# Kernel optimization log

Hardware: AMD Instinct MI355X
Metric: run time of the kernel (lower is better)

Reference implementation:

```python
import jax, jax.numpy as jnp
import numpy as np

N_NODES = 100000
N_EDGES = 1600000
IN_DIM = 33
HID = 128
N_CLASSES = 10
N_GRAPHS = 128


def _glorot(key, shape):
    fan_in, fan_out = shape[0], shape[1]
    lim = (6.0 / (fan_in + fan_out)) ** 0.5
    return jax.random.uniform(key, shape, jnp.float32, -lim, lim)


def setup_inputs() -> dict:
    key = jax.random.key(0)
    ks = jax.random.split(key, 20)
    x = jax.random.normal(ks[0], (N_NODES, IN_DIM), jnp.float32)
    edge_index = jax.random.randint(ks[1], (2, N_EDGES), 0, N_NODES, jnp.int64)
    edge_w = jax.random.uniform(ks[2], (N_EDGES,), jnp.float32)
    batch = jnp.sort(jax.random.randint(ks[3], (N_NODES,), 0, N_GRAPHS, jnp.int64))
    p = {
        "We": _glorot(ks[4], (IN_DIM, HID)), "be": jnp.zeros((HID,), jnp.float32),
        "W1": _glorot(ks[5], (HID, HID)), "b1": jnp.zeros((HID,), jnp.float32),
        "W2": _glorot(ks[6], (HID, HID)), "b2": jnp.zeros((HID,), jnp.float32),
        "W3": _glorot(ks[7], (HID, HID)), "b3": jnp.zeros((HID,), jnp.float32),
        "W4": _glorot(ks[8], (HID, HID)), "b4": jnp.zeros((HID,), jnp.float32),
        "Wr1": _glorot(ks[9], (HID, HID // 2)), "br1": jnp.zeros((HID // 2,), jnp.float32),
        "Wr2": _glorot(ks[10], (HID // 2, HID // 4)), "br2": jnp.zeros((HID // 4,), jnp.float32),
        "Wr3": _glorot(ks[11], (HID // 4, N_CLASSES)),
    }
    return dict(x=x, edge_index=edge_index, edge_w=edge_w, batch=batch, **p)


def reference(x, edge_index, edge_w, batch,
              We, be, W1, b1, W2, b2, W3, b3, W4, b4,
              Wr1, br1, Wr2, br2, Wr3):
    N = x.shape[0]
    row, col = edge_index[0], edge_index[1]
    # PyG gcn_norm with add_self_loops=True: append (i,i) edges with weight 1
    loop = jnp.arange(N)
    row2 = jnp.concatenate([row, loop])
    col2 = jnp.concatenate([col, loop])
    w2 = jnp.concatenate([edge_w, jnp.ones((N,), edge_w.dtype)])
    deg = jax.ops.segment_sum(w2, col2, num_segments=N)  # in-degree incl. self-loop
    dinv = jnp.where(deg > 0, deg ** -0.5, 0.0)
    norm = dinv[row2] * w2 * dinv[col2]  # [E+N] symmetric normalization

    def conv(h, W, b):
        h = h @ W  # linear transform first (PyG GCNConv)
        msg = norm[:, None] * h[row2]  # gather + scale
        return jax.ops.segment_sum(msg, col2, num_segments=N) + b  # scatter-add to targets

    h = x @ We + be
    h = jax.nn.relu(conv(h, W1, b1))
    h = jax.nn.relu(conv(h, W2, b2))
    h = jax.nn.relu(conv(h, W3, b3))
    h = jax.nn.relu(conv(h, W4, b4))

    # global mean pool over graphs
    sums = jax.ops.segment_sum(h, batch, num_segments=N_GRAPHS)
    cnt = jax.ops.segment_sum(jnp.ones((N,), h.dtype), batch, num_segments=N_GRAPHS)
    pooled = sums / jnp.maximum(cnt, 1.0)[:, None]  # [G, HID]

    r = jax.nn.relu(pooled @ Wr1 + br1)
    r = jax.nn.relu(r @ Wr2 + br2)
    return r @ Wr3  # [G, n_classes]
```

## Files before the change

kernel.cpp:

```cpp
#include <hip/hip_runtime.h>
#include <hip/hip_bf16.h>

#define NN 100000
#define NE 1600000
#define IN_DIM 33
#define HID 128
#define NG 128
#define NCLS 10

using short8 = __attribute__((ext_vector_type(8))) short;
using floatx4 = __attribute__((ext_vector_type(4))) float;

static __device__ __forceinline__ size_t szmul(int a, int b) {
    return (size_t)a * (size_t)b;
}

static __device__ __forceinline__ unsigned short f2bf(float f) {
    unsigned u = __float_as_uint(f);
    u += 0x7fffu + ((u >> 16) & 1u);
    return (unsigned short)(u >> 16);
}
static __device__ __forceinline__ float bf_lo(unsigned u) { return __uint_as_float(u << 16); }
static __device__ __forceinline__ float bf_hi(unsigned u) { return __uint_as_float(u & 0xffff0000u); }

__global__ void k_init(int* bucket_cnt, int* bucket_fill, float* gsum) {
    int i = blockIdx.x * blockDim.x + threadIdx.x;
    if (i < 513) { bucket_cnt[i] = 0; bucket_fill[i] = 0; }
    if (i < NG * HID) gsum[i] = 0.0f;
}


__global__ __launch_bounds__(256) void k_bhist(const int* __restrict__ col,
                                               int* __restrict__ bucket_cnt, int e, int nbk) {
    __shared__ int hist[512];
    int tid = threadIdx.x;
    for (int i = tid; i < nbk; i += 256) hist[i] = 0;
    __syncthreads();
    for (int i = blockIdx.x * 256 + tid; i < e; i += 256 * 256)
        atomicAdd(&hist[col[i] >> 8], 1);
    __syncthreads();
    for (int i = tid; i < nbk; i += 256)
        if (hist[i]) atomicAdd(&bucket_cnt[i], hist[i]);
}

__global__ void k_scan_small(int* data, int nb) {
    __shared__ int s[512];
    int t = threadIdx.x;
    int v = (t < nb) ? data[t] : 0;
    s[t] = v;
    __syncthreads();
    for (int o = 1; o < 512; o <<= 1) {
        int a = (t >= o) ? s[t - o] : 0;
        __syncthreads();
        s[t] += a;
        __syncthreads();
    }
    if (t < nb) data[t] = s[t] - v;
    if (t == nb - 1) data[nb] = s[t];
}

__global__ __launch_bounds__(256) void k_bin_scatter(const int* __restrict__ row,
                                                     const int* __restrict__ col,
                                                     const float* __restrict__ w,
                                                     const int* __restrict__ bucket_base,
                                                     int* __restrict__ bucket_fill,
                                                     uint2* __restrict__ binned, int e, int nbk) {
    __shared__ int hist[512], rnk[512], basub[512];
    int tid = threadIdx.x;
    int c0 = blockIdx.x * 4096;
    for (int i = tid; i < nbk; i += 256) { hist[i] = 0; rnk[i] = 0; }
    __syncthreads();
    int myb[16]; unsigned myp[16]; unsigned myw[16];
#pragma unroll
    for (int u = 0; u < 16; ++u) {
        int idx = c0 + u * 256 + tid;
        int b = -1;
        if (idx < e) {
            int c = col[idx];
            int r = row[idx];
            myw[u] = __float_as_uint(w[idx]);
            b = c >> 8;
            myp[u] = ((unsigned)(c & 255) << 17) | (unsigned)r;
            atomicAdd(&hist[b], 1);
        }
        myb[u] = b;
    }
    __syncthreads();
    for (int i = tid; i < nbk; i += 256) {
        int c = hist[i];
        basub[i] = (c > 0) ? (bucket_base[i] + atomicAdd(&bucket_fill[i], c)) : 0;
    }
    __syncthreads();
#pragma unroll
    for (int u = 0; u < 16; ++u) {
        int b = myb[u];
        if (b >= 0) {
            int rk = atomicAdd(&rnk[b], 1);
            binned[basub[b] + rk] = make_uint2(myp[u], myw[u]);
        }
    }
}

__global__ __launch_bounds__(256) void k_bucket_cnt(const uint2* __restrict__ binned,
                                                    const int* __restrict__ bucket_base,
                                                    int* __restrict__ cnt,
                                                    float* __restrict__ wsum, int n) {
    __shared__ int c256[256];
    __shared__ float s256[256];
    int b = blockIdx.x, tid = threadIdx.x;
    c256[tid] = 0;
    s256[tid] = 0.0f;
    __syncthreads();
    int beg = bucket_base[b], end = bucket_base[b + 1];
    for (int e2 = beg + tid; e2 < end; e2 += 256) {
        uint2 rec = binned[e2];
        int lo = (rec.x >> 17) & 255;
        atomicAdd(&c256[lo], 1);
        atomicAdd(&s256[lo], __uint_as_float(rec.y));
    }
    __syncthreads();
    int node = b * 256 + tid;
    if (node < n) { cnt[node] = c256[tid]; wsum[node] = s256[tid]; }
}

__global__ void k_dinv(float* __restrict__ dinv, float* __restrict__ selfn, int n) {
    int i = blockIdx.x * blockDim.x + threadIdx.x;
    if (i >= n) return;
    float d = 1.0f + dinv[i];
    float di = (d > 0.0f) ? (1.0f / sqrtf(d)) : 0.0f;
    dinv[i] = di;
    selfn[i] = di * di;
}

#define SCAN_B 1024
__global__ void k_scan1(const int* __restrict__ cnt, int* __restrict__ rowptr,
                        int* __restrict__ bsums, int n) {
    __shared__ int s[SCAN_B];
    int t = threadIdx.x;
    int i = blockIdx.x * SCAN_B + t;
    int v = (i < n) ? cnt[i] : 0;
    s[t] = v;
    __syncthreads();
    for (int o = 1; o < SCAN_B; o <<= 1) {
        int a = (t >= o) ? s[t - o] : 0;
        __syncthreads();
        s[t] += a;
        __syncthreads();
    }
    if (i < n) rowptr[i] = s[t] - v;
    if (t == SCAN_B - 1) bsums[blockIdx.x] = s[t];
}

__global__ void k_scan3(int* rowptr, const int* __restrict__ bsums, int n, int etot) {
    int i = blockIdx.x * blockDim.x + threadIdx.x;
    if (i < n) rowptr[i] += bsums[i >> 10];
    else if (i == n) rowptr[n] = etot;
}

__global__ __launch_bounds__(256) void k_bucket_scatter(const uint2* __restrict__ binned,
                                                        const int* __restrict__ bucket_base,
                                                        const int* __restrict__ rowptr,
                                                        const float* __restrict__ dinv,
                                                        int2* __restrict__ csr, int n) {
    __shared__ int f256[256];
    int b = blockIdx.x, tid = threadIdx.x;
    f256[tid] = 0;
    __syncthreads();
    int beg = bucket_base[b], end = bucket_base[b + 1];
    for (int e2 = beg + tid; e2 < end; e2 += 256) {
        uint2 rec = binned[e2];
        int lo = (rec.x >> 17) & 255;
        int node = (b << 8) | lo;
        int src = rec.x & 0x1FFFF;
        float nw = dinv[src] * __uint_as_float(rec.y) * dinv[node];
        int pos = rowptr[node] + atomicAdd(&f256[lo], 1);
        csr[pos] = make_int2(src, __float_as_int(nw));
    }
    (void)n;
}

__global__ void k_combine(const float* __restrict__ We, const float* __restrict__ W1,
                          const float* __restrict__ be,
                          float* __restrict__ M, float* __restrict__ v) {
    int f = threadIdx.x;
    int k = blockIdx.x;
    if (k < IN_DIM) {
        float a = 0.0f;
#pragma unroll 8
        for (int j = 0; j < HID; ++j) a += We[k * HID + j] * W1[j * HID + f];
        M[k * HID + f] = a;
    } else {
        float a = 0.0f;
#pragma unroll 8
        for (int j = 0; j < HID; ++j) a += be[j] * W1[j * HID + f];
        v[f] = a;
    }
}

__global__ void k_wcast3(const float* __restrict__ W1, const float* __restrict__ W2,
                         const float* __restrict__ W3, unsigned short* __restrict__ Wt) {
    int k = blockIdx.x, c = threadIdx.x, l = blockIdx.y;
    const float* W = (l == 0) ? W1 : (l == 1) ? W2 : W3;
    Wt[((size_t)l * HID + c) * HID + k] = f2bf(W[k * HID + c]);
}

__global__ __launch_bounds__(256) void k_gemm_x(const float* __restrict__ x,
                                                const float* __restrict__ M,
                                                const float* __restrict__ v,
                                                unsigned short* __restrict__ tb, int n) {
    __shared__ float sX[32 * IN_DIM];
    int n0 = blockIdx.x * 32;
    int tid = threadIdx.x;
    int cnt = n - n0; if (cnt > 32) cnt = 32;
    for (int idx = tid; idx < cnt * IN_DIM; idx += 256)
        sX[idx] = x[szmul(n0, IN_DIM) + idx];
    __syncthreads();
    int f = tid & 127, g = tid >> 7;
    float Mc[IN_DIM];
#pragma unroll
    for (int k = 0; k < IN_DIM; ++k) Mc[k] = M[k * HID + f];
    float vf = v[f];
    int ndEnd = g * 16 + 16; if (ndEnd > cnt) ndEnd = cnt;
    for (int nd = g * 16; nd < ndEnd; ++nd) {
        float a = vf;
#pragma unroll
        for (int k = 0; k < IN_DIM; ++k) a += sX[nd * IN_DIM + k] * Mc[k];
        tb[szmul(n0 + nd, HID) + f] = f2bf(a);
    }
}

__global__ __launch_bounds__(256) void k_gemm_mfma(const unsigned short* __restrict__ A,
                                                   const unsigned short* __restrict__ Wt,
                                                   unsigned short* __restrict__ T, int n) {
    int wave = threadIdx.x >> 6;
    int lane = threadIdx.x & 63;
    int r = lane & 15, kg = lane >> 4;
    int row0 = blockIdx.x * 64 + wave * 16;
    int arow = row0 + r;
    short8 af[4];
#pragma unroll
    for (int kk = 0; kk < 4; ++kk) {
        if (arow < n)
            af[kk] = *reinterpret_cast<const short8*>(A + szmul(arow, HID) + kk * 32 + kg * 8);
        else
            af[kk] = short8{0, 0, 0, 0, 0, 0, 0, 0};
    }
    floatx4 acc[8];
#pragma unroll
    for (int ct = 0; ct < 8; ++ct) acc[ct] = floatx4{0.f, 0.f, 0.f, 0.f};
#pragma unroll
    for (int kk = 0; kk < 4; ++kk) {
#pragma unroll
        for (int ct = 0; ct < 8; ++ct) {
            short8 bf = *reinterpret_cast<const short8*>(
                Wt + (size_t)(ct * 16 + r) * HID + kk * 32 + kg * 8);
            acc[ct] = __builtin_amdgcn_mfma_f32_16x16x32_bf16(af[kk], bf, acc[ct], 0, 0, 0);
        }
    }
#pragma unroll
    for (int ct = 0; ct < 8; ++ct) {
#pragma unroll
        for (int reg = 0; reg < 4; ++reg) {
            int orow = row0 + kg * 4 + reg;
            if (orow < n)
                T[szmul(orow, HID) + ct * 16 + r] = f2bf(acc[ct][reg]);
        }
    }
}

__global__ __launch_bounds__(256) void k_aggregate(const uint4* __restrict__ tb,
                                                   const int* __restrict__ rowptr,
                                                   const int2* __restrict__ csr,
                                                   const float* __restrict__ selfn,
                                                   const float* __restrict__ bias,
                                                   uint4* __restrict__ hout, int n) {
    int i = (blockIdx.x * 256 + threadIdx.x) >> 4;
    if (i >= n) return;
    int p = threadIdx.x & 15;
    uint4 sv = tb[szmul(i, 16) + p];
    float sn = selfn[i];
    const float4* bp = reinterpret_cast<const float4*>(bias + p * 8);
    float4 b0 = bp[0], b1 = bp[1];
    float a0 = b0.x + sn * bf_lo(sv.x), a1 = b0.y + sn * bf_hi(sv.x);
    float a2 = b0.z + sn * bf_lo(sv.y), a3 = b0.w + sn * bf_hi(sv.y);
    float a4 = b1.x + sn * bf_lo(sv.z), a5 = b1.y + sn * bf_hi(sv.z);
    float a6 = b1.z + sn * bf_lo(sv.w), a7 = b1.w + sn * bf_hi(sv.w);
    int beg = rowptr[i], end = rowptr[i + 1];
#pragma unroll 4
    for (int j = beg; j < end; ++j) {
        int2 e = csr[j];
        float wj = __int_as_float(e.y);
        uint4 r = tb[szmul(e.x, 16) + p];
        a0 += wj * bf_lo(r.x); a1 += wj * bf_hi(r.x);
        a2 += wj * bf_lo(r.y); a3 += wj * bf_hi(r.y);
        a4 += wj * bf_lo(r.z); a5 += wj * bf_hi(r.z);
        a6 += wj * bf_lo(r.w); a7 += wj * bf_hi(r.w);
    }
    unsigned u0 = (unsigned)f2bf(fmaxf(a0, 0.f)) | ((unsigned)f2bf(fmaxf(a1, 0.f)) << 16);
    unsigned u1 = (unsigned)f2bf(fmaxf(a2, 0.f)) | ((unsigned)f2bf(fmaxf(a3, 0.f)) << 16);
    unsigned u2 = (unsigned)f2bf(fmaxf(a4, 0.f)) | ((unsigned)f2bf(fmaxf(a5, 0.f)) << 16);
    unsigned u3 = (unsigned)f2bf(fmaxf(a6, 0.f)) | ((unsigned)f2bf(fmaxf(a7, 0.f)) << 16);
    hout[szmul(i, 16) + p] = make_uint4(u0, u1, u2, u3);
}

__global__ void k_gcount_bs(const int* __restrict__ batch, int* gcnt, int n) {
    int g = threadIdx.x;
    if (g >= NG) return;
    int lo = 0, hi = n;
    while (lo < hi) { int mid = (lo + hi) >> 1; if (batch[mid] < g) lo = mid + 1; else hi = mid; }
    int start = lo;
    lo = 0; hi = n;
    while (lo < hi) { int mid = (lo + hi) >> 1; if (batch[mid] < g + 1) lo = mid + 1; else hi = mid; }
    gcnt[g] = lo - start;
}

__global__ __launch_bounds__(128) void k_pool(const unsigned short* __restrict__ h,
                                              const int* __restrict__ batch,
                                              float* gsum, int n) {
    int f = threadIdx.x;
    int i0 = blockIdx.x * 32;
    int i1 = min(i0 + 32, n);
    if (i0 >= n) return;
    float acc = 0.0f;
    int cur = batch[i0];
    for (int i = i0; i < i1; ++i) {
        int g = batch[i];
        if (g != cur) { atomicAdd(&gsum[cur * HID + f], acc); acc = 0.0f; cur = g; }
        acc += __uint_as_float((unsigned)h[szmul(i, HID) + f] << 16);
    }
    atomicAdd(&gsum[cur * HID + f], acc);
}

__global__ __launch_bounds__(128) void k_mlp(const float* __restrict__ gsum,
                                             const int* __restrict__ gcnt,
                                             const float* __restrict__ Wr1, const float* __restrict__ br1,
                                             const float* __restrict__ Wr2, const float* __restrict__ br2,
                                             const float* __restrict__ Wr3,
                                             float* __restrict__ out) {
    int g = blockIdx.x;
    int t = threadIdx.x;
    __shared__ float p[HID];
    __shared__ float r1[64];
    __shared__ float r2[32];
    float c = fmaxf((float)gcnt[g], 1.0f);
    p[t] = gsum[g * HID + t] / c;
    __syncthreads();
    if (t < 64) {
        float a = br1[t];
#pragma unroll 8
        for (int k = 0; k < HID; ++k) a += p[k] * Wr1[k * 64 + t];
        r1[t] = fmaxf(a, 0.0f);
    }
    __syncthreads();
    if (t < 32) {
        float a = br2[t];
#pragma unroll 8
        for (int k = 0; k < 64; ++k) a += r1[k] * Wr2[k * 32 + t];
        r2[t] = fmaxf(a, 0.0f);
    }
    __syncthreads();
    if (t < NCLS) {
        float a = 0.0f;
#pragma unroll
        for (int k = 0; k < 32; ++k) a += r2[k] * Wr3[k * NCLS + t];
        out[g * NCLS + t] = a;
    }
}

extern "C" void kernel_launch(void* const* d_in, const int* in_sizes, int n_in,
                              void* d_out, int out_size, void* d_ws, size_t ws_size,
                              hipStream_t stream) {
    const float* x     = (const float*)d_in[0];
    const int*   ei    = (const int*)d_in[1];
    const float* ew    = (const float*)d_in[2];
    const int*   batch = (const int*)d_in[3];
    const float* We  = (const float*)d_in[4];
    const float* be  = (const float*)d_in[5];
    const float* Wl[4] = { (const float*)d_in[6], (const float*)d_in[8],
                           (const float*)d_in[10], (const float*)d_in[12] };
    const float* bl[4] = { (const float*)d_in[7], (const float*)d_in[9],
                           (const float*)d_in[11], (const float*)d_in[13] };
    const float* Wr1 = (const float*)d_in[14];
    const float* br1 = (const float*)d_in[15];
    const float* Wr2 = (const float*)d_in[16];
    const float* br2 = (const float*)d_in[17];
    const float* Wr3 = (const float*)d_in[18];
    float* out = (float*)d_out;

    const int N = in_sizes[3];
    const int E = in_sizes[2];
    const int* row = ei;
    const int* col = ei + E;
    const int nbk = (N + 255) >> 8;

    char* w = (char*)d_ws;
    size_t off = 0;
    auto alloc = [&](size_t bytes) -> void* {
        void* p = w + off;
        off = (off + bytes + 255) & ~(size_t)255;
        return p;
    };
    float* dinv       = (float*)alloc((size_t)N * 4);
    float* selfn      = (float*)alloc((size_t)N * 4);
    int*   cnt        = (int*)  alloc((size_t)N * 4);
    int*   rowptr     = (int*)  alloc((size_t)(N + 1) * 4);
    int*   bsums      = (int*)  alloc(4096);
    int*   bucket_cnt = (int*)  alloc(513 * 4);
    int*   bucket_fill= (int*)  alloc(513 * 4);
    int2*  csr        = (int2*) alloc((size_t)E * 8);
    unsigned short* h  = (unsigned short*)alloc((size_t)N * HID * 2);
    unsigned short* tb = (unsigned short*)alloc((size_t)N * HID * 2);
    unsigned short* Wt = (unsigned short*)alloc((size_t)3 * HID * HID * 2);
    float* M          = (float*)alloc((size_t)IN_DIM * HID * 4);
    float* vbe        = (float*)alloc((size_t)HID * 4);
    float* gsum       = (float*)alloc((size_t)NG * HID * 4);
    int*   gcnt       = (int*)  alloc((size_t)NG * 4);
    uint2* binned     = (uint2*)tb;
    (void)ws_size;

    auto cdiv = [](int a, int b) { return (a + b - 1) / b; };

    k_init<<<64, 256, 0, stream>>>(bucket_cnt, bucket_fill, gsum);
    k_bhist<<<256, 256, 0, stream>>>(col, bucket_cnt, E, nbk);
    k_scan_small<<<1, 512, 0, stream>>>(bucket_cnt, nbk);
    k_bin_scatter<<<cdiv(E, 4096), 256, 0, stream>>>(row, col, ew, bucket_cnt,
                                                     bucket_fill, binned, E, nbk);
    k_bucket_cnt<<<nbk, 256, 0, stream>>>(binned, bucket_cnt, cnt, dinv, N);
    k_dinv<<<cdiv(N, 256), 256, 0, stream>>>(dinv, selfn, N);

    int nb = cdiv(N, SCAN_B);
    k_scan1<<<nb, SCAN_B, 0, stream>>>(cnt, rowptr, bsums, N);
    k_scan_small<<<1, 512, 0, stream>>>(bsums, nb);
    k_scan3<<<cdiv(N + 1, 256), 256, 0, stream>>>(rowptr, bsums, N, E);
    k_bucket_scatter<<<nbk, 256, 0, stream>>>(binned, bucket_cnt, rowptr, dinv, csr, N);

    k_combine<<<IN_DIM + 1, HID, 0, stream>>>(We, Wl[0], be, M, vbe);
    k_wcast3<<<dim3(HID, 3), HID, 0, stream>>>(Wl[1], Wl[2], Wl[3], Wt);

    k_gemm_x<<<cdiv(N, 32), 256, 0, stream>>>(x, M, vbe, tb, N);
    k_aggregate<<<cdiv(N, 16), 256, 0, stream>>>((const uint4*)tb, rowptr, csr,
                                                 selfn, bl[0], (uint4*)h, N);

    for (int l = 1; l < 4; ++l) {
        k_gemm_mfma<<<cdiv(N, 64), 256, 0, stream>>>(h, Wt + (size_t)(l - 1) * HID * HID,
                                                     tb, N);
        k_aggregate<<<cdiv(N, 16), 256, 0, stream>>>((const uint4*)tb, rowptr, csr,
                                                     selfn, bl[l], (uint4*)h, N);
    }

    k_gcount_bs<<<1, 128, 0, stream>>>(batch, gcnt, N);
    k_pool<<<cdiv(N, 32), 128, 0, stream>>>(h, batch, gsum, N);
    k_mlp<<<NG, HID, 0, stream>>>(gsum, gcnt, Wr1, br1, Wr2, br2, Wr3, out);

    (void)out_size; (void)n_in;
}
```

Before: 500.7 us.

## Store node features in feature-sliced layout so aggregation gathers per slice

Node feature buffers move from row-major [N,128] to eight slices of [N,16] bf16. The aggregation kernel now gives each block one slice, with two threads per node covering 16 features, so the random gathers for a slice touch a 3.2MB region that fits better in cache. The GEMM, pooling and input-projection kernels are rewritten to read and write the sliced layout. The trade-off is that CSR indices and weights are read eight times instead of once, and each gather becomes a 32-byte segment rather than a full 256-byte row.

```diff
diff --git a/kernel.cpp b/kernel.cpp
--- a/kernel.cpp
+++ b/kernel.cpp
@@ -204,6 +204,7 @@
     Wt[((size_t)l * HID + c) * HID + k] = f2bf(W[k * HID + c]);
 }
 
+
 __global__ __launch_bounds__(256) void k_gemm_x(const float* __restrict__ x,
                                                 const float* __restrict__ M,
                                                 const float* __restrict__ v,
@@ -220,12 +221,13 @@
 #pragma unroll
     for (int k = 0; k < IN_DIM; ++k) Mc[k] = M[k * HID + f];
     float vf = v[f];
+    size_t sbase = ((size_t)(f >> 4) * n) * 16 + (f & 15);
     int ndEnd = g * 16 + 16; if (ndEnd > cnt) ndEnd = cnt;
     for (int nd = g * 16; nd < ndEnd; ++nd) {
         float a = vf;
 #pragma unroll
         for (int k = 0; k < IN_DIM; ++k) a += sX[nd * IN_DIM + k] * Mc[k];
-        tb[szmul(n0 + nd, HID) + f] = f2bf(a);
+        tb[sbase + (size_t)(n0 + nd) * 16] = f2bf(a);
     }
 }
 
@@ -240,8 +242,11 @@
     short8 af[4];
 #pragma unroll
     for (int kk = 0; kk < 4; ++kk) {
+        int f0 = kk * 32 + kg * 8;
+        int sl = f0 >> 4, pp = (f0 >> 3) & 1;
         if (arow < n)
-            af[kk] = *reinterpret_cast<const short8*>(A + szmul(arow, HID) + kk * 32 + kg * 8);
+            af[kk] = *reinterpret_cast<const short8*>(
+                A + ((size_t)sl * n + arow) * 16 + pp * 8);
         else
             af[kk] = short8{0, 0, 0, 0, 0, 0, 0, 0};
     }
@@ -263,7 +268,7 @@
         for (int reg = 0; reg < 4; ++reg) {
             int orow = row0 + kg * 4 + reg;
             if (orow < n)
-                T[szmul(orow, HID) + ct * 16 + r] = f2bf(acc[ct][reg]);
+                T[((size_t)ct * n + orow) * 16 + r] = f2bf(acc[ct][reg]);
         }
     }
 }
@@ -274,13 +279,16 @@
                                                    const float* __restrict__ selfn,
                                                    const float* __restrict__ bias,
                                                    uint4* __restrict__ hout, int n) {
-    int i = (blockIdx.x * 256 + threadIdx.x) >> 4;
+    int s = blockIdx.x & 7;
+    int i = (blockIdx.x >> 3) * 128 + (threadIdx.x >> 1);
     if (i >= n) return;
-    int p = threadIdx.x & 15;
-    uint4 sv = tb[szmul(i, 16) + p];
+    int p = threadIdx.x & 1;
+    const uint4* tbs = tb + (size_t)s * n * 2;
+    uint4 sv = tbs[(size_t)i * 2 + p];
     float sn = selfn[i];
-    const float4* bp = reinterpret_cast<const float4*>(bias + p * 8);
-    float4 b0 = bp[0], b1 = bp[1];
+    const float* bb = bias + s * 16 + p * 8;
+    float4 b0 = *reinterpret_cast<const float4*>(bb);
+    float4 b1 = *reinterpret_cast<const float4*>(bb + 4);
     float a0 = b0.x + sn * bf_lo(sv.x), a1 = b0.y + sn * bf_hi(sv.x);
     float a2 = b0.z + sn * bf_lo(sv.y), a3 = b0.w + sn * bf_hi(sv.y);
     float a4 = b1.x + sn * bf_lo(sv.z), a5 = b1.y + sn * bf_hi(sv.z);
@@ -290,7 +298,7 @@
     for (int j = beg; j < end; ++j) {
         int2 e = csr[j];
         float wj = __int_as_float(e.y);
-        uint4 r = tb[szmul(e.x, 16) + p];
+        uint4 r = tbs[(size_t)e.x * 2 + p];
         a0 += wj * bf_lo(r.x); a1 += wj * bf_hi(r.x);
         a2 += wj * bf_lo(r.y); a3 += wj * bf_hi(r.y);
         a4 += wj * bf_lo(r.z); a5 += wj * bf_hi(r.z);
@@ -300,7 +308,7 @@
     unsigned u1 = (unsigned)f2bf(fmaxf(a2, 0.f)) | ((unsigned)f2bf(fmaxf(a3, 0.f)) << 16);
     unsigned u2 = (unsigned)f2bf(fmaxf(a4, 0.f)) | ((unsigned)f2bf(fmaxf(a5, 0.f)) << 16);
     unsigned u3 = (unsigned)f2bf(fmaxf(a6, 0.f)) | ((unsigned)f2bf(fmaxf(a7, 0.f)) << 16);
-    hout[szmul(i, 16) + p] = make_uint4(u0, u1, u2, u3);
+    hout[(size_t)s * n * 2 + (size_t)i * 2 + p] = make_uint4(u0, u1, u2, u3);
 }
 
 __global__ void k_gcount_bs(const int* __restrict__ batch, int* gcnt, int n) {
@@ -321,12 +329,13 @@
     int i0 = blockIdx.x * 32;
     int i1 = min(i0 + 32, n);
     if (i0 >= n) return;
+    size_t sbase = ((size_t)(f >> 4) * n) * 16 + (f & 15);
     float acc = 0.0f;
     int cur = batch[i0];
     for (int i = i0; i < i1; ++i) {
         int g = batch[i];
         if (g != cur) { atomicAdd(&gsum[cur * HID + f], acc); acc = 0.0f; cur = g; }
-        acc += __uint_as_float((unsigned)h[szmul(i, HID) + f] << 16);
+        acc += __uint_as_float((unsigned)h[sbase + (size_t)i * 16] << 16);
     }
     atomicAdd(&gsum[cur * HID + f], acc);
 }
@@ -437,15 +446,17 @@
     k_combine<<<IN_DIM + 1, HID, 0, stream>>>(We, Wl[0], be, M, vbe);
     k_wcast3<<<dim3(HID, 3), HID, 0, stream>>>(Wl[1], Wl[2], Wl[3], Wt);
 
+    int agg_grid = cdiv(N, 128) * 8;
+
     k_gemm_x<<<cdiv(N, 32), 256, 0, stream>>>(x, M, vbe, tb, N);
-    k_aggregate<<<cdiv(N, 16), 256, 0, stream>>>((const uint4*)tb, rowptr, csr,
-                                                 selfn, bl[0], (uint4*)h, N);
+    k_aggregate<<<agg_grid, 256, 0, stream>>>((const uint4*)tb, rowptr, csr,
+                                              selfn, bl[0], (uint4*)h, N);
 
     for (int l = 1; l < 4; ++l) {
         k_gemm_mfma<<<cdiv(N, 64), 256, 0, stream>>>(h, Wt + (size_t)(l - 1) * HID * HID,
                                                      tb, N);
-        k_aggregate<<<cdiv(N, 16), 256, 0, stream>>>((const uint4*)tb, rowptr, csr,
-                                                     selfn, bl[l], (uint4*)h, N);
+        k_aggregate<<<agg_grid, 256, 0, stream>>>((const uint4*)tb, rowptr, csr,
+                                                  selfn, bl[l], (uint4*)h, N);
     }
 
     k_gcount_bs<<<1, 128, 0, stream>>>(batch, gcnt, N);
```

Result: slower. 666.9 us (+33.2%).
